# Kernel tuning notes

Measured on AMD Instinct MI355X. Metric: run time of the kernel, lower is better.

The kernel has to match this reference:

```python
import jax, jax.numpy as jnp
import numpy as np

B, M, E, R, U, I = 4096, 100, 128, 64, 100000, 100000


def setup_inputs() -> dict:
    key = jax.random.key(0)
    ks = jax.random.split(key, 10)
    return {
        "user_id": jax.random.randint(ks[0], (B,), 0, U),
        "item_id_p": jax.random.randint(ks[1], (B,), 0, I),
        "item_id_n": jax.random.randint(ks[2], (B,), 0, I),
        "inter_id": jax.random.randint(ks[3], (B, M), 0, I),
        "user_emb_w": jax.random.normal(ks[4], (U, E), jnp.float32),
        "item_emb_w": jax.random.normal(ks[5], (I, E), jnp.float32),
        "ua_key": jax.random.normal(ks[6], (R, E), jnp.float32),
        "ua_val": jax.random.normal(ks[7], (R, E), jnp.float32),
        "ia_key": jax.random.normal(ks[8], (R, E), jnp.float32),
        "ia_val": jax.random.normal(ks[9], (R, E), jnp.float32),
    }


def _maxnorm_lookup(w, ids, max_norm=1.0, eps=1e-7):
    # torch nn.Embedding(max_norm=1): rows with norm > max_norm are renormalized
    v = w[ids]
    n = jnp.linalg.norm(v, axis=-1, keepdims=True)
    scale = jnp.where(n > max_norm, max_norm / (n + eps), jnp.ones_like(n))
    return v * scale


def _rel_attn(key_w, val_w, mul_feat, attn_feat, inter):
    # w = key*val elementwise (R,E); einsum 'mbj,ij->bmj' sums w over relations
    wsum = jnp.sum(key_w * val_w, axis=0)                 # (E,)
    rel = mul_feat[:, None, :] * inter * wsum             # (B,M,E) rel_vecs
    logits = jnp.einsum("bme,be->bm", rel, attn_feat)      # (B,M)
    attn = jax.nn.softmax(logits, axis=1)
    return jnp.einsum("bm,bme->be", attn, rel)             # (B,E)


def reference(user_id, item_id_p, item_id_n, inter_id,
              user_emb_w, item_emb_w, ua_key, ua_val, ia_key, ia_val):
    u = _maxnorm_lookup(user_emb_w, user_id)
    ip = _maxnorm_lookup(item_emb_w, item_id_p)
    inn = _maxnorm_lookup(item_emb_w, item_id_n)
    inter = _maxnorm_lookup(item_emb_w, inter_id)
    # UserAttention: rel from item*inter, softmax vs user
    # ItemAttention (model_type='plus'): rel from user*inter, softmax vs item
    rel_p = _rel_attn(ua_key, ua_val, ip, u, inter) + _rel_attn(ia_key, ia_val, u, ip, inter)
    rel_n = _rel_attn(ua_key, ua_val, inn, u, inter) + _rel_attn(ia_key, ia_val, u, inn, inter)
    return (u, ip, inn, rel_p, rel_n)
```

## Files before the change

kernel.cpp:

```cpp
#include <hip/hip_runtime.h>
#include <math.h>

#define BB 4096
#define MM 100
#define EE 128
#define RR 64

typedef float v4f __attribute__((ext_vector_type(4)));
typedef float v2f __attribute__((ext_vector_type(2)));

__device__ __forceinline__ v4f ld4v(const float* p) {
    return *reinterpret_cast<const v4f*>(p);
}
__device__ __forceinline__ void st4v(float* p, v4f v) {
    *reinterpret_cast<v4f*>(p) = v;
}
__device__ __forceinline__ float pdot8(v4f a, v4f qa, v4f b, v4f qb) {
    v2f acc = a.xy * qa.xy;
    acc += a.zw * qa.zw;
    acc += b.xy * qb.xy;
    acc += b.zw * qb.zw;
    return acc.x + acc.y;
}
__device__ __forceinline__ v4f v4red(v4f a, int off) {
    a.x += __shfl_xor(a.x, off, 64); a.y += __shfl_xor(a.y, off, 64);
    a.z += __shfl_xor(a.z, off, 64); a.w += __shfl_xor(a.w, off, 64);
    return a;
}
__device__ __forceinline__ v4f relcomb(v4f x1, v4f w1, v4f S1v, float i1,
                                       v4f x2, v4f w2, v4f S2v, float i2) {
    return x1 * w1 * (S1v * i1) + x2 * w2 * (S2v * i2);
}

template<int CTRL>
__device__ __forceinline__ float dpp_add(float x) {
    int y = __builtin_amdgcn_update_dpp(0, __float_as_int(x), CTRL, 0xF, 0xF, true);
    return x + __int_as_float(y);
}
__device__ __forceinline__ float row16_allreduce(float x) {
    x = dpp_add<0x121>(x);
    x = dpp_add<0x122>(x);
    x = dpp_add<0x124>(x);
    x = dpp_add<0x128>(x);
    return x;
}

__global__ __launch_bounds__(512)
void wsum_kernel(const float* __restrict__ ua_key, const float* __restrict__ ua_val,
                 const float* __restrict__ ia_key, const float* __restrict__ ia_val,
                 float* __restrict__ ws) {
    __shared__ float part[4][EE];
    const float* k = (blockIdx.x == 0) ? ua_key : ia_key;
    const float* v = (blockIdx.x == 0) ? ua_val : ia_val;
    int e = threadIdx.x & 127;
    int q = threadIdx.x >> 7;
    float s = 0.f;
    #pragma unroll
    for (int j = 0; j < 16; ++j) {
        int r = q * 16 + j;
        s += k[r * EE + e] * v[r * EE + e];
    }
    part[q][e] = s;
    __syncthreads();
    if (threadIdx.x < EE)
        ws[blockIdx.x * EE + e] = part[0][e] + part[1][e] + part[2][e] + part[3][e];
}

__global__ __launch_bounds__(64)
void hlrm_main(const int* __restrict__ user_id,
               const int* __restrict__ ip_id,
               const int* __restrict__ in_id,
               const int* __restrict__ inter_id,
               const float* __restrict__ user_w,
               const float* __restrict__ item_w,
               const float* __restrict__ ws,
               float* __restrict__ out) {
    __shared__ int sw[MM];

    const int b    = blockIdx.x;
    const int lane = threadIdx.x;
    const int g    = lane >> 4;
    const int hl   = lane & 15;
    const int e0   = hl * 4;

    const int* ib = inter_id + b * MM;
    int sid0 = ib[g],      sid1 = ib[4 + g],  sid2 = ib[8 + g],
        sid3 = ib[12 + g], sid4 = ib[16 + g];

    v4f va0, vb0, va1, vb1, va2, vb2, va3, vb3, va4, vb4;
#define LOADT(J) do {                                             \
        const float* pt = item_w + ((uint)sid##J << 7) + e0;      \
        va##J = ld4v(pt);                                         \
        vb##J = ld4v(pt + 64);                                    \
    } while (0)
    LOADT(0); LOADT(1); LOADT(2); LOADT(3); LOADT(4);

    if (lane < 50)
        *reinterpret_cast<int2*>(sw + 2 * lane) =
            *reinterpret_cast<const int2*>(ib + 2 * lane);

    int uid = user_id[b], pid = ip_id[b], nid = in_id[b];
    const float* pu = user_w + ((uint)uid << 7);
    const float* pp = item_w + ((uint)pid << 7);
    const float* pn = item_w + ((uint)nid << 7);
    v4f ru_a = ld4v(pu + e0), ru_b = ld4v(pu + e0 + 64);
    v4f rp_a = ld4v(pp + e0), rp_b = ld4v(pp + e0 + 64);
    v4f rn_a = ld4v(pn + e0), rn_b = ld4v(pn + e0 + 64);
    v4f waa = ld4v(ws + e0),       wab = ld4v(ws + e0 + 64);
    v4f wia = ld4v(ws + 128 + e0), wib = ld4v(ws + 192 + e0);

    float ssu = pdot8(ru_a, ru_a, ru_b, ru_b);
    float ssp = pdot8(rp_a, rp_a, rp_b, rp_b);
    float ssn = pdot8(rn_a, rn_a, rn_b, rn_b);
    ssu = row16_allreduce(ssu);
    ssp = row16_allreduce(ssp);
    ssn = row16_allreduce(ssn);
    float scu = (ssu > 1.f) ? __builtin_amdgcn_rsqf(ssu) : 1.f;
    float scp = (ssp > 1.f) ? __builtin_amdgcn_rsqf(ssp) : 1.f;
    float scn = (ssn > 1.f) ? __builtin_amdgcn_rsqf(ssn) : 1.f;

    float cup = scu * scp, cun = scu * scn;
    v4f qa0 = ru_a * rp_a * waa * cup, qb0 = ru_b * rp_b * wab * cup;
    v4f qa1 = ru_a * rp_a * wia * cup, qb1 = ru_b * rp_b * wib * cup;
    v4f qa2 = ru_a * rn_a * waa * cun, qb2 = ru_b * rn_b * wab * cun;
    v4f qa3 = ru_a * rn_a * wia * cun, qb3 = ru_b * rn_b * wib * cun;

    v4f Sa0 = {0,0,0,0}, Sa1 = {0,0,0,0}, Sa2 = {0,0,0,0}, Sa3 = {0,0,0,0};
    v4f Sb0 = {0,0,0,0}, Sb1 = {0,0,0,0}, Sb2 = {0,0,0,0}, Sb3 = {0,0,0,0};
    float den0 = 0.f, den1 = 0.f, den2 = 0.f, den3 = 0.f;

    sid0 = sw[20 + g]; sid1 = sw[24 + g]; sid2 = sw[28 + g];
    sid3 = sw[32 + g]; sid4 = sw[36 + g];

#define STEP(J) do {                                                        \
        float ss = pdot8(va##J, va##J, vb##J, vb##J);                       \
        float d0 = pdot8(va##J, qa0, vb##J, qb0);                           \
        float d1 = pdot8(va##J, qa1, vb##J, qb1);                           \
        float d2 = pdot8(va##J, qa2, vb##J, qb2);                           \
        float d3 = pdot8(va##J, qa3, vb##J, qb3);                           \
        ss = row16_allreduce(ss);                                           \
        d0 = row16_allreduce(d0); d1 = row16_allreduce(d1);                 \
        d2 = row16_allreduce(d2); d3 = row16_allreduce(d3);                 \
        float sc = (ss > 1.f) ? __builtin_amdgcn_rsqf(ss) : 1.f;            \
        float w0 = __expf(d0 * sc), w1 = __expf(d1 * sc);                   \
        float w2 = __expf(d2 * sc), w3 = __expf(d3 * sc);                   \
        den0 += w0; den1 += w1; den2 += w2; den3 += w3;                     \
        w0 *= sc; w1 *= sc; w2 *= sc; w3 *= sc;                             \
        Sa0 += va##J * w0; Sb0 += vb##J * w0;                               \
        Sa1 += va##J * w1; Sb1 += vb##J * w1;                               \
        Sa2 += va##J * w2; Sb2 += vb##J * w2;                               \
        Sa3 += va##J * w3; Sb3 += vb##J * w3;                               \
    } while (0)

    #pragma unroll 1
    for (int it = 0; it < 4; ++it) {
        STEP(0); LOADT(0);
        STEP(1); LOADT(1);
        STEP(2); LOADT(2);
        STEP(3); LOADT(3);
        STEP(4); LOADT(4);
        if (it < 3) {
            int o = 20 * it + 40 + g;
            sid0 = sw[o];      sid1 = sw[o + 4];  sid2 = sw[o + 8];
            sid3 = sw[o + 12]; sid4 = sw[o + 16];
        }
    }
    STEP(0); STEP(1); STEP(2); STEP(3); STEP(4);
#undef STEP
#undef LOADT

    #pragma unroll
    for (int off = 16; off < 64; off <<= 1) {
        Sa0 = v4red(Sa0, off); Sb0 = v4red(Sb0, off);
        Sa1 = v4red(Sa1, off); Sb1 = v4red(Sb1, off);
        Sa2 = v4red(Sa2, off); Sb2 = v4red(Sb2, off);
        Sa3 = v4red(Sa3, off); Sb3 = v4red(Sb3, off);
        den0 += __shfl_xor(den0, off, 64);
        den1 += __shfl_xor(den1, off, 64);
        den2 += __shfl_xor(den2, off, 64);
        den3 += __shfl_xor(den3, off, 64);
    }
    float iD0 = 1.f / den0, iD1 = 1.f / den1, iD2 = 1.f / den2, iD3 = 1.f / den3;

    const float* qu = user_w + ((uint)uid << 7);
    const float* qp = item_w + ((uint)pid << 7);
    const float* qn = item_w + ((uint)nid << 7);
    v4f u_a = ld4v(qu + e0) * scu,      u_b = ld4v(qu + e0 + 64) * scu;
    v4f p_a = ld4v(qp + e0) * scp,      p_b = ld4v(qp + e0 + 64) * scp;
    v4f n_a = ld4v(qn + e0) * scn,      n_b = ld4v(qn + e0 + 64) * scn;
    v4f w0a = ld4v(ws + e0),            w0b = ld4v(ws + e0 + 64);
    v4f w1a = ld4v(ws + 128 + e0),      w1b = ld4v(ws + 192 + e0);

    size_t base = (size_t)b * EE;
    const size_t P = (size_t)BB * EE;
    if (g == 0) {
        v4f ra = relcomb(p_a, w0a, Sa0, iD0, u_a, w1a, Sa1, iD1);
        v4f rb = relcomb(p_b, w0b, Sb0, iD0, u_b, w1b, Sb1, iD1);
        st4v(out + 3 * P + base + e0, ra);
        st4v(out + 3 * P + base + e0 + 64, rb);
    } else if (g == 1) {
        v4f ra = relcomb(n_a, w0a, Sa2, iD2, u_a, w1a, Sa3, iD3);
        v4f rb = relcomb(n_b, w0b, Sb2, iD2, u_b, w1b, Sb3, iD3);
        st4v(out + 4 * P + base + e0, ra);
        st4v(out + 4 * P + base + e0 + 64, rb);
    } else if (g == 2) {
        st4v(out + 0 * P + base + e0, u_a);
        st4v(out + 0 * P + base + e0 + 64, u_b);
        st4v(out + 1 * P + base + e0, p_a);
        st4v(out + 1 * P + base + e0 + 64, p_b);
    } else {
        st4v(out + 2 * P + base + e0, n_a);
        st4v(out + 2 * P + base + e0 + 64, n_b);
    }
}

extern "C" void kernel_launch(void* const* d_in, const int* in_sizes, int n_in,
                              void* d_out, int out_size, void* d_ws, size_t ws_size,
                              hipStream_t stream) {
    const int*   user_id   = (const int*)d_in[0];
    const int*   item_id_p = (const int*)d_in[1];
    const int*   item_id_n = (const int*)d_in[2];
    const int*   inter_id  = (const int*)d_in[3];
    const float* user_w    = (const float*)d_in[4];
    const float* item_w    = (const float*)d_in[5];
    const float* ua_key    = (const float*)d_in[6];
    const float* ua_val    = (const float*)d_in[7];
    const float* ia_key    = (const float*)d_in[8];
    const float* ia_val    = (const float*)d_in[9];
    float* out = (float*)d_out;
    float* ws  = (float*)d_ws;

    wsum_kernel<<<2, 512, 0, stream>>>(ua_key, ua_val, ia_key, ia_val, ws);
    hlrm_main<<<BB, 64, 0, stream>>>(user_id, item_id_p, item_id_n, inter_id,
                                     user_w, item_w, ws, out);
}
```

Measured before the change: 43.26 us.

## Convert item table to fp16 per call and gather half-precision rows

Adds a kernel that converts the whole item embedding table to fp16 in the workspace on each call. The main kernel then gathers the 100 interaction rows per batch element as fp16 and widens them in registers, halving gather bytes. In exchange it reads and writes the full table every call and loses precision in the interaction rows. If the workspace is too small it falls back to the original fp32 kernel.

```diff
diff --git a/kernel.cpp b/kernel.cpp
--- a/kernel.cpp
+++ b/kernel.cpp
@@ -1,4 +1,5 @@
 #include <hip/hip_runtime.h>
+#include <hip/hip_fp16.h>
 #include <math.h>
 
 #define BB 4096
@@ -8,6 +9,7 @@
 
 typedef float v4f __attribute__((ext_vector_type(4)));
 typedef float v2f __attribute__((ext_vector_type(2)));
+typedef int   v4i __attribute__((ext_vector_type(4)));
 
 __device__ __forceinline__ v4f ld4v(const float* p) {
     return *reinterpret_cast<const v4f*>(p);
@@ -66,15 +68,33 @@
         ws[blockIdx.x * EE + e] = part[0][e] + part[1][e] + part[2][e] + part[3][e];
 }
 
+struct h8 { __half2 a, b, c, d; };
+__global__ __launch_bounds__(256)
+void cvt_kernel(const float* __restrict__ item_w, __half* __restrict__ hw, int nchunk) {
+    int idx = blockIdx.x * 256 + threadIdx.x;
+    if (idx >= nchunk) return;
+    int row = idx >> 4, i = idx & 15;
+    const float* src = item_w + ((size_t)row << 7);
+    v4f lo = ld4v(src + i * 4);
+    v4f hi = ld4v(src + 64 + i * 4);
+    h8 o;
+    o.a = __floats2half2_rn(lo.x, lo.y);
+    o.b = __floats2half2_rn(lo.z, lo.w);
+    o.c = __floats2half2_rn(hi.x, hi.y);
+    o.d = __floats2half2_rn(hi.z, hi.w);
+    *reinterpret_cast<h8*>(hw + ((size_t)row << 7) + i * 8) = o;
+}
+
 __global__ __launch_bounds__(64)
-void hlrm_main(const int* __restrict__ user_id,
-               const int* __restrict__ ip_id,
-               const int* __restrict__ in_id,
-               const int* __restrict__ inter_id,
-               const float* __restrict__ user_w,
-               const float* __restrict__ item_w,
-               const float* __restrict__ ws,
-               float* __restrict__ out) {
+void hlrm_main16(const int* __restrict__ user_id,
+                 const int* __restrict__ ip_id,
+                 const int* __restrict__ in_id,
+                 const int* __restrict__ inter_id,
+                 const float* __restrict__ user_w,
+                 const float* __restrict__ item_w,
+                 const __half* __restrict__ hwt,
+                 const float* __restrict__ ws,
+                 float* __restrict__ out) {
     __shared__ int sw[MM];
 
     const int b    = blockIdx.x;
@@ -87,11 +107,10 @@
     int sid0 = ib[g],      sid1 = ib[4 + g],  sid2 = ib[8 + g],
         sid3 = ib[12 + g], sid4 = ib[16 + g];
 
-    v4f va0, vb0, va1, vb1, va2, vb2, va3, vb3, va4, vb4;
-#define LOADT(J) do {                                             \
-        const float* pt = item_w + ((uint)sid##J << 7) + e0;      \
-        va##J = ld4v(pt);                                         \
-        vb##J = ld4v(pt + 64);                                    \
+    v4i t0, t1, t2, t3, t4;
+#define LOADT(J) do {                                                     \
+        t##J = *reinterpret_cast<const v4i*>(                             \
+            hwt + (((size_t)(uint)sid##J) << 7) + (hl << 3));             \
     } while (0)
     LOADT(0); LOADT(1); LOADT(2); LOADT(3); LOADT(4);
 
@@ -133,11 +152,19 @@
     sid3 = sw[32 + g]; sid4 = sw[36 + g];
 
 #define STEP(J) do {                                                        \
-        float ss = pdot8(va##J, va##J, vb##J, vb##J);                       \
-        float d0 = pdot8(va##J, qa0, vb##J, qb0);                           \
-        float d1 = pdot8(va##J, qa1, vb##J, qb1);                           \
-        float d2 = pdot8(va##J, qa2, vb##J, qb2);                           \
-        float d3 = pdot8(va##J, qa3, vb##J, qb3);                           \
+        union { v4i iv; __half2 h[4]; } u_;                                 \
+        u_.iv = t##J;                                                       \
+        float2 l0_ = __half22float2(u_.h[0]);                               \
+        float2 l1_ = __half22float2(u_.h[1]);                               \
+        float2 h0_ = __half22float2(u_.h[2]);                               \
+        float2 h1_ = __half22float2(u_.h[3]);                               \
+        v4f va = {l0_.x, l0_.y, l1_.x, l1_.y};                              \
+        v4f vb = {h0_.x, h0_.y, h1_.x, h1_.y};                              \
+        float ss = pdot8(va, va, vb, vb);                                   \
+        float d0 = pdot8(va, qa0, vb, qb0);                                 \
+        float d1 = pdot8(va, qa1, vb, qb1);                                 \
+        float d2 = pdot8(va, qa2, vb, qb2);                                 \
+        float d3 = pdot8(va, qa3, vb, qb3);                                 \
         ss = row16_allreduce(ss);                                           \
         d0 = row16_allreduce(d0); d1 = row16_allreduce(d1);                 \
         d2 = row16_allreduce(d2); d3 = row16_allreduce(d3);                 \
@@ -146,10 +173,10 @@
         float w2 = __expf(d2 * sc), w3 = __expf(d3 * sc);                   \
         den0 += w0; den1 += w1; den2 += w2; den3 += w3;                     \
         w0 *= sc; w1 *= sc; w2 *= sc; w3 *= sc;                             \
-        Sa0 += va##J * w0; Sb0 += vb##J * w0;                               \
-        Sa1 += va##J * w1; Sb1 += vb##J * w1;                               \
-        Sa2 += va##J * w2; Sb2 += vb##J * w2;                               \
-        Sa3 += va##J * w3; Sb3 += vb##J * w3;                               \
+        Sa0 += va * w0; Sb0 += vb * w0;                                     \
+        Sa1 += va * w1; Sb1 += vb * w1;                                     \
+        Sa2 += va * w2; Sb2 += vb * w2;                                     \
+        Sa3 += va * w3; Sb3 += vb * w3;                                     \
     } while (0)
 
     #pragma unroll 1
@@ -214,6 +241,153 @@
     }
 }
 
+__global__ __launch_bounds__(64)
+void hlrm_main32(const int* __restrict__ user_id,
+                 const int* __restrict__ ip_id,
+                 const int* __restrict__ in_id,
+                 const int* __restrict__ inter_id,
+                 const float* __restrict__ user_w,
+                 const float* __restrict__ item_w,
+                 const float* __restrict__ ws,
+                 float* __restrict__ out) {
+    __shared__ int sw[MM];
+    const int b    = blockIdx.x;
+    const int lane = threadIdx.x;
+    const int g    = lane >> 4;
+    const int hl   = lane & 15;
+    const int e0   = hl * 4;
+
+    const int* ib = inter_id + b * MM;
+    int sid0 = ib[g],      sid1 = ib[4 + g],  sid2 = ib[8 + g],
+        sid3 = ib[12 + g], sid4 = ib[16 + g];
+
+    v4f va0, vb0, va1, vb1, va2, vb2, va3, vb3, va4, vb4;
+#define LOADT(J) do {                                             \
+        const float* pt = item_w + ((uint)sid##J << 7) + e0;      \
+        va##J = ld4v(pt);                                         \
+        vb##J = ld4v(pt + 64);                                    \
+    } while (0)
+    LOADT(0); LOADT(1); LOADT(2); LOADT(3); LOADT(4);
+
+    if (lane < 50)
+        *reinterpret_cast<int2*>(sw + 2 * lane) =
+            *reinterpret_cast<const int2*>(ib + 2 * lane);
+
+    int uid = user_id[b], pid = ip_id[b], nid = in_id[b];
+    const float* pu = user_w + ((uint)uid << 7);
+    const float* pp = item_w + ((uint)pid << 7);
+    const float* pn = item_w + ((uint)nid << 7);
+    v4f ru_a = ld4v(pu + e0), ru_b = ld4v(pu + e0 + 64);
+    v4f rp_a = ld4v(pp + e0), rp_b = ld4v(pp + e0 + 64);
+    v4f rn_a = ld4v(pn + e0), rn_b = ld4v(pn + e0 + 64);
+    v4f waa = ld4v(ws + e0),       wab = ld4v(ws + e0 + 64);
+    v4f wia = ld4v(ws + 128 + e0), wib = ld4v(ws + 192 + e0);
+
+    float ssu = pdot8(ru_a, ru_a, ru_b, ru_b);
+    float ssp = pdot8(rp_a, rp_a, rp_b, rp_b);
+    float ssn = pdot8(rn_a, rn_a, rn_b, rn_b);
+    ssu = row16_allreduce(ssu);
+    ssp = row16_allreduce(ssp);
+    ssn = row16_allreduce(ssn);
+    float scu = (ssu > 1.f) ? __builtin_amdgcn_rsqf(ssu) : 1.f;
+    float scp = (ssp > 1.f) ? __builtin_amdgcn_rsqf(ssp) : 1.f;
+    float scn = (ssn > 1.f) ? __builtin_amdgcn_rsqf(ssn) : 1.f;
+
+    float cup = scu * scp, cun = scu * scn;
+    v4f qa0 = ru_a * rp_a * waa * cup, qb0 = ru_b * rp_b * wab * cup;
+    v4f qa1 = ru_a * rp_a * wia * cup, qb1 = ru_b * rp_b * wib * cup;
+    v4f qa2 = ru_a * rn_a * waa * cun, qb2 = ru_b * rn_b * wab * cun;
+    v4f qa3 = ru_a * rn_a * wia * cun, qb3 = ru_b * rn_b * wib * cun;
+
+    v4f Sa0 = {0,0,0,0}, Sa1 = {0,0,0,0}, Sa2 = {0,0,0,0}, Sa3 = {0,0,0,0};
+    v4f Sb0 = {0,0,0,0}, Sb1 = {0,0,0,0}, Sb2 = {0,0,0,0}, Sb3 = {0,0,0,0};
+    float den0 = 0.f, den1 = 0.f, den2 = 0.f, den3 = 0.f;
+
+    sid0 = sw[20 + g]; sid1 = sw[24 + g]; sid2 = sw[28 + g];
+    sid3 = sw[32 + g]; sid4 = sw[36 + g];
+
+#define STEP(J) do {                                                        \
+        float ss = pdot8(va##J, va##J, vb##J, vb##J);                       \
+        float d0 = pdot8(va##J, qa0, vb##J, qb0);                           \
+        float d1 = pdot8(va##J, qa1, vb##J, qb1);                           \
+        float d2 = pdot8(va##J, qa2, vb##J, qb2);                           \
+        float d3 = pdot8(va##J, qa3, vb##J, qb3);                           \
+        ss = row16_allreduce(ss);                                           \
+        d0 = row16_allreduce(d0); d1 = row16_allreduce(d1);                 \
+        d2 = row16_allreduce(d2); d3 = row16_allreduce(d3);                 \
+        float sc = (ss > 1.f) ? __builtin_amdgcn_rsqf(ss) : 1.f;            \
+        float w0 = __expf(d0 * sc), w1 = __expf(d1 * sc);                   \
+        float w2 = __expf(d2 * sc), w3 = __expf(d3 * sc);                   \
+        den0 += w0; den1 += w1; den2 += w2; den3 += w3;                     \
+        w0 *= sc; w1 *= sc; w2 *= sc; w3 *= sc;                             \
+        Sa0 += va##J * w0; Sb0 += vb##J * w0;                               \
+        Sa1 += va##J * w1; Sb1 += vb##J * w1;                               \
+        Sa2 += va##J * w2; Sb2 += vb##J * w2;                               \
+        Sa3 += va##J * w3; Sb3 += vb##J * w3;                               \
+    } while (0)
+
+    #pragma unroll 1
+    for (int it = 0; it < 4; ++it) {
+        STEP(0); LOADT(0);
+        STEP(1); LOADT(1);
+        STEP(2); LOADT(2);
+        STEP(3); LOADT(3);
+        STEP(4); LOADT(4);
+        if (it < 3) {
+            int o = 20 * it + 40 + g;
+            sid0 = sw[o];      sid1 = sw[o + 4];  sid2 = sw[o + 8];
+            sid3 = sw[o + 12]; sid4 = sw[o + 16];
+        }
+    }
+    STEP(0); STEP(1); STEP(2); STEP(3); STEP(4);
+#undef STEP
+#undef LOADT
+
+    #pragma unroll
+    for (int off = 16; off < 64; off <<= 1) {
+        Sa0 = v4red(Sa0, off); Sb0 = v4red(Sb0, off);
+        Sa1 = v4red(Sa1, off); Sb1 = v4red(Sb1, off);
+        Sa2 = v4red(Sa2, off); Sb2 = v4red(Sb2, off);
+        Sa3 = v4red(Sa3, off); Sb3 = v4red(Sb3, off);
+        den0 += __shfl_xor(den0, off, 64);
+        den1 += __shfl_xor(den1, off, 64);
+        den2 += __shfl_xor(den2, off, 64);
+        den3 += __shfl_xor(den3, off, 64);
+    }
+    float iD0 = 1.f / den0, iD1 = 1.f / den1, iD2 = 1.f / den2, iD3 = 1.f / den3;
+
+    const float* qu = user_w + ((uint)uid << 7);
+    const float* qp = item_w + ((uint)pid << 7);
+    const float* qn = item_w + ((uint)nid << 7);
+    v4f u_a = ld4v(qu + e0) * scu,      u_b = ld4v(qu + e0 + 64) * scu;
+    v4f p_a = ld4v(qp + e0) * scp,      p_b = ld4v(qp + e0 + 64) * scp;
+    v4f n_a = ld4v(qn + e0) * scn,      n_b = ld4v(qn + e0 + 64) * scn;
+    v4f w0a = ld4v(ws + e0),            w0b = ld4v(ws + e0 + 64);
+    v4f w1a = ld4v(ws + 128 + e0),      w1b = ld4v(ws + 192 + e0);
+
+    size_t base = (size_t)b * EE;
+    const size_t P = (size_t)BB * EE;
+    if (g == 0) {
+        v4f ra = relcomb(p_a, w0a, Sa0, iD0, u_a, w1a, Sa1, iD1);
+        v4f rb = relcomb(p_b, w0b, Sb0, iD0, u_b, w1b, Sb1, iD1);
+        st4v(out + 3 * P + base + e0, ra);
+        st4v(out + 3 * P + base + e0 + 64, rb);
+    } else if (g == 1) {
+        v4f ra = relcomb(n_a, w0a, Sa2, iD2, u_a, w1a, Sa3, iD3);
+        v4f rb = relcomb(n_b, w0b, Sb2, iD2, u_b, w1b, Sb3, iD3);
+        st4v(out + 4 * P + base + e0, ra);
+        st4v(out + 4 * P + base + e0 + 64, rb);
+    } else if (g == 2) {
+        st4v(out + 0 * P + base + e0, u_a);
+        st4v(out + 0 * P + base + e0 + 64, u_b);
+        st4v(out + 1 * P + base + e0, p_a);
+        st4v(out + 1 * P + base + e0 + 64, p_b);
+    } else {
+        st4v(out + 2 * P + base + e0, n_a);
+        st4v(out + 2 * P + base + e0 + 64, n_b);
+    }
+}
+
 extern "C" void kernel_launch(void* const* d_in, const int* in_sizes, int n_in,
                               void* d_out, int out_size, void* d_ws, size_t ws_size,
                               hipStream_t stream) {
@@ -230,7 +404,19 @@
     float* out = (float*)d_out;
     float* ws  = (float*)d_ws;
 
+    const int I = in_sizes[5] / EE;
+    const size_t need = 1024 + (size_t)I * EE * sizeof(__half);
+
     wsum_kernel<<<2, 512, 0, stream>>>(ua_key, ua_val, ia_key, ia_val, ws);
-    hlrm_main<<<BB, 64, 0, stream>>>(user_id, item_id_p, item_id_n, inter_id,
-                                     user_w, item_w, ws, out);
-}
+
+    if (ws_size >= need) {
+        __half* hw = reinterpret_cast<__half*>((char*)d_ws + 1024);
+        int nchunk = I * 16;
+        cvt_kernel<<<(nchunk + 255) / 256, 256, 0, stream>>>(item_w, hw, nchunk);
+        hlrm_main16<<<BB, 64, 0, stream>>>(user_id, item_id_p, item_id_n, inter_id,
+                                           user_w, item_w, hw, ws, out);
+    } else {
+        hlrm_main32<<<BB, 64, 0, stream>>>(user_id, item_id_p, item_id_n, inter_id,
+                                           user_w, item_w, ws, out);
+    }
+}
```

Measured after the change: 48.51 us. 12.1% more time.
